# Performance work log

Hardware: AMD Instinct MI355X
Metric: run time of the kernel (lower is better)

## Reference

```python
import jax, jax.numpy as jnp
import numpy as np

NEG_INF = -1e30
EPS = 1e-7  # keras epsilon used by K.ctc_batch_cost


def setup_inputs() -> dict:
    key = jax.random.key(0)
    k1, k2 = jax.random.split(key)
    B, T, C, L = 1024, 256, 128, 32
    logits = jax.random.normal(k1, (B, T, C), dtype=jnp.float32)
    y_pred = jax.nn.softmax(logits, axis=-1)  # ctc_batch_cost expects probabilities
    y_true = jax.random.randint(k2, (B, L), 0, 126, dtype=jnp.int64)
    return {"y_true": y_true, "y_pred": y_pred}


def _ctc_batch_cost(y_true, y_pred):
    # Faithful to K.ctc_batch_cost with input_length=T, label_length=L, blank=C-1
    B, T, C = y_pred.shape
    L = y_true.shape[1]
    blank = C - 1
    S = 2 * L + 1
    logp = jnp.log(y_pred + EPS)  # [B,T,C]

    # extended label sequence: blank, l0, blank, l1, ..., blank  -> [B,S]
    ext = jnp.full((B, S), blank, dtype=jnp.int32)
    ext = ext.at[:, 1::2].set(y_true.astype(jnp.int32))

    # emission log-probs along extended labels: [B,T,S]
    lp_ext = jnp.take_along_axis(logp, ext[:, None, :], axis=2)

    # s-2 skip allowed only for non-blank labels differing from label two back
    is_blank = ext == blank
    same2 = jnp.concatenate(
        [jnp.ones((B, 2), bool), ext[:, 2:] == ext[:, :-2]], axis=1)
    skip_add = jnp.where(is_blank | same2, NEG_INF, 0.0)  # [B,S]

    alpha0 = jnp.full((B, S), NEG_INF, dtype=logp.dtype)
    alpha0 = alpha0.at[:, 0].set(lp_ext[:, 0, 0])
    alpha0 = alpha0.at[:, 1].set(lp_ext[:, 0, 1])

    def shift(x, n):
        return jnp.pad(x, ((0, 0), (n, 0)), constant_values=NEG_INF)[:, :S]

    def step(alpha, lp_t):
        a0 = alpha
        a1 = shift(alpha, 1)
        a2 = jnp.maximum(shift(alpha, 2) + skip_add, NEG_INF)
        m = jnp.maximum(jnp.maximum(a0, a1), a2)
        lse = m + jnp.log(jnp.exp(a0 - m) + jnp.exp(a1 - m) + jnp.exp(a2 - m))
        new = jnp.maximum(lse + lp_t, NEG_INF)
        return new, None

    lp_ext_t = jnp.swapaxes(lp_ext, 0, 1)  # [T,B,S]
    alpha_T, _ = jax.lax.scan(step, alpha0, lp_ext_t[1:])
    final = jnp.logaddexp(alpha_T[:, S - 1], alpha_T[:, S - 2])  # [B]
    return -final[:, None]  # [B,1] like ctc_batch_cost


def reference(y_true, y_pred):
    return _ctc_batch_cost(y_true, y_pred)
```

## Files before the change

kernel.cpp:

```cpp
#include <hip/hip_runtime.h>
#include <hip/hip_bf16.h>


#define CTC_B 1024
#define CTC_T 256
#define CTC_C 128
#define CTC_L 32
#define CTC_BLANK 127
#define CTC_EPS 1e-7f

#define KSTRIDE 130
#define TABSZ  (34 * KSTRIDE)

#define DPP_WAVE_SHL1 0x130
#define DPP_WAVE_SHR1 0x138

__device__ __forceinline__ double bperm_f64(int addr, double v) {
    union { double d; int i[2]; } u; u.d = v;
    int x = __builtin_amdgcn_ds_bpermute(addr, u.i[0]);
    int y = __builtin_amdgcn_ds_bpermute(addr, u.i[1]);
    union { int i[2]; double d; } r; r.i[0] = x; r.i[1] = y;
    return r.d;
}

__device__ __forceinline__ double dpp_shr1_f64(double v) {
    union { double d; int i[2]; } u; u.d = v;
    int x = __builtin_amdgcn_update_dpp(0, u.i[0], DPP_WAVE_SHR1, 0xF, 0xF, true);
    int y = __builtin_amdgcn_update_dpp(0, u.i[1], DPP_WAVE_SHR1, 0xF, 0xF, true);
    union { int i[2]; double d; } r; r.i[0] = x; r.i[1] = y;
    return r.d;
}

__device__ __forceinline__ double dpp_shl1_f64(double v) {
    union { double d; int i[2]; } u; u.d = v;
    int x = __builtin_amdgcn_update_dpp(0, u.i[0], DPP_WAVE_SHL1, 0xF, 0xF, true);
    int y = __builtin_amdgcn_update_dpp(0, u.i[1], DPP_WAVE_SHL1, 0xF, 0xF, true);
    union { int i[2]; double d; } r; r.i[0] = x; r.i[1] = y;
    return r.d;
}

__device__ __forceinline__ double bcast0_f64(double v) {
    union { double d; int i[2]; } u; u.d = v;
    int x = __builtin_amdgcn_readfirstlane(u.i[0]);
    int y = __builtin_amdgcn_readfirstlane(u.i[1]);
    union { int i[2]; double d; } r; r.i[0] = x; r.i[1] = y;
    return r.d;
}

__global__ __launch_bounds__(256) void ctc_loss_kernel(
    const int* __restrict__ y_true,
    const float* __restrict__ y_pred,
    float* __restrict__ out)
{
    __shared__ float tabs[2 * TABSZ];
    float* Ftab = tabs;
    float* Btab = tabs + TABSZ;

    const int b = blockIdx.x;
    const int tid = threadIdx.x;
    const int lane = tid & 63;
    const int wave = tid >> 6;

    const float* yp = y_pred + (size_t)b * CTC_T * CTC_C;

    int lbl = CTC_BLANK;
    if (lane < CTC_L) lbl = y_true[b * CTC_L + lane];

    {
        const int t0 = wave * 64;
        const int src_addr = (lbl >> 1) << 2;
        const bool odd = (lbl & 1) != 0;
        float* tab = (wave < 2) ? Ftab : Btab;
        #pragma unroll 8
        for (int k = 0; k < 64; ++k) {
            const int t = t0 + k;
            const float2 r =
                *reinterpret_cast<const float2*>(yp + (size_t)t * CTC_C + 2 * lane);
            union { float f; int i; } c0, c1;
            c0.f = r.x; c1.f = r.y;
            int g0 = __builtin_amdgcn_ds_bpermute(src_addr, c0.i);
            int g1 = __builtin_amdgcn_ds_bpermute(src_addr, c1.i);
            union { int i; float f; } s0, s1;
            s0.i = g0; s1.i = g1;
            float p = odd ? s1.f : s0.f;
            float v = (lane == 33) ? 0.0f : (p + CTC_EPS) * 128.0f;
            const int idx = (wave < 2) ? ((t + 127) & 127) : (255 - t);
            if (lane <= 33) tab[lane * KSTRIDE + idx] = v;
        }
    }
    __syncthreads();

    if (wave != 0) return;

    double skip = 0.0;
    if (lane >= 1 && lane < CTC_L) {
        if (y_true[b * CTC_L + lane - 1] != lbl) skip = 1.0;
    }
    double skipn = 0.0;
    if (lane <= 30) {
        if (y_true[b * CTC_L + lane + 1] != lbl) skipn = 1.0;
    } else if (lane == 32) {
        skipn = 1.0;
    }

    const int lidx = (lane < 32) ? lane : 32;
    const int pv_idx = (lane < 32) ? lane : 33;
    const int tn = (lane <= 30) ? (lane + 1)
                 : (lane == 31) ? 33
                 : (lane == 32) ? 0
                 : 32;
    const int pbi = (lane == 32) ? 33 : 32;
    const bool is32 = (lane == 32);

    const float* Fpv = Ftab + pv_idx * KSTRIDE;
    const float* Fpb = Ftab + 32 * KSTRIDE;
    const float* Bpa = Btab + lidx * KSTRIDE;
    const float* Bp1 = Btab + tn * KSTRIDE;
    const float* Bpb = Btab + pbi * KSTRIDE;

    double lo = 0.0, hi = 0.0;
    if (lane == 0) {
        lo = (double)Ftab[32 * KSTRIDE + 127];
        hi = (double)Ftab[0 * KSTRIDE + 127];
    }
    double a = 0.0, bb = 0.0;
    if (lane == 31) { a = 1.0; bb = 1.0; }

#define STEP(pvf, pbf, paf, pa1f, pbbf) {                       \
        double ph  = dpp_shr1_f64(hi);                          \
        double a1s = dpp_shl1_f64(a);                           \
        double a1  = is32 ? bcast0_f64(a) : a1s;                \
        double nl = (lo + ph) * (double)(pbf);                  \
        double nh = (hi + lo + skip * ph) * (double)(pvf);      \
        double v  = (double)(pa1f) * a1;                        \
        double u  = (double)(pbbf) * bb;                        \
        double nb = u + v;                                      \
        double na = fma((double)(paf), a, fma(skipn, v, u));    \
        lo = nl; hi = nh; a = na; bb = nb;                      \
    }

#define LD2(p, o) (*reinterpret_cast<const float2*>((p) + (o)))

    float2 c_pv0 = LD2(Fpv, 0), c_pv1 = LD2(Fpv, 2);
    float2 c_pb0 = LD2(Fpb, 0), c_pb1 = LD2(Fpb, 2);
    float2 c_pa0 = LD2(Bpa, 0), c_pa1 = LD2(Bpa, 2);
    float2 c_p10 = LD2(Bp1, 0), c_p11 = LD2(Bp1, 2);
    float2 c_pb0b = LD2(Bpb, 0), c_pb1b = LD2(Bpb, 2);

    for (int g = 0; g < 31; ++g) {
        const int o = 4 * (g + 1);
        float2 n_pv0 = LD2(Fpv, o), n_pv1 = LD2(Fpv, o + 2);
        float2 n_pb0 = LD2(Fpb, o), n_pb1 = LD2(Fpb, o + 2);
        float2 n_pa0 = LD2(Bpa, o), n_pa1 = LD2(Bpa, o + 2);
        float2 n_p10 = LD2(Bp1, o), n_p11 = LD2(Bp1, o + 2);
        float2 n_pb0b = LD2(Bpb, o), n_pb1b = LD2(Bpb, o + 2);

        STEP(c_pv0.x, c_pb0.x, c_pa0.x, c_p10.x, c_pb0b.x);
        STEP(c_pv0.y, c_pb0.y, c_pa0.y, c_p10.y, c_pb0b.y);
        STEP(c_pv1.x, c_pb1.x, c_pa1.x, c_p11.x, c_pb1b.x);
        STEP(c_pv1.y, c_pb1.y, c_pa1.y, c_p11.y, c_pb1b.y);

        c_pv0 = n_pv0; c_pv1 = n_pv1;
        c_pb0 = n_pb0; c_pb1 = n_pb1;
        c_pa0 = n_pa0; c_pa1 = n_pa1;
        c_p10 = n_p10; c_p11 = n_p11;
        c_pb0b = n_pb0b; c_pb1b = n_pb1b;
    }

    STEP(c_pv0.x, c_pb0.x, c_pa0.x, c_p10.x, c_pb0b.x);
    STEP(c_pv0.y, c_pb0.y, c_pa0.y, c_p10.y, c_pb0b.y);
    STEP(c_pv1.x, c_pb1.x, c_pa1.x, c_p11.x, c_pb1b.x);

    {
        double a1s = dpp_shl1_f64(a);
        double a1  = is32 ? bcast0_f64(a) : a1s;
        double v  = (double)c_p11.y * a1;
        double u  = (double)c_pb1b.y * bb;
        double nb = u + v;
        double na = fma((double)c_pa1.y, a, fma(skipn, v, u));
        a = na; bb = nb;
    }

#undef STEP
#undef LD2

    double beA = bperm_f64(32 << 2, a);
    double beB = bperm_f64(((lane + 63) & 63) << 2, bb);
    double be = (lane == 0) ? beA : beB;
    double partial = (lane <= 32) ? (lo * be + hi * a) : 0.0;
    #pragma unroll
    for (int off = 32; off >= 1; off >>= 1)
        partial += __shfl_down(partial, off);
    if (lane == 0) {
        out[b] = (float)(1242.1197475634219 - log(partial));
    }
}

extern "C" void kernel_launch(void* const* d_in, const int* in_sizes, int n_in,
                              void* d_out, int out_size, void* d_ws, size_t ws_size,
                              hipStream_t stream) {
    const int*   y_true = (const int*)d_in[0];
    const float* y_pred = (const float*)d_in[1];
    float*       out    = (float*)d_out;

    ctc_loss_kernel<<<CTC_B, 256, 0, stream>>>(y_true, y_pred, out);
}
```

Baseline: 212.5 us.

## Split CTC into gather kernel and 64-thread scan kernel via workspace

Splits the fused kernel in two. The first kernel gathers the label emission probabilities into a global workspace, using two blocks per batch item. The second kernel runs the forward/backward recurrence with one 64-thread wave per batch item and reads its probabilities from global memory (L2) instead of LDS. The aim is to stop three idle waves holding a block's LDS during the serial scan, raise occupancy, and overlap the scan across more batches. The cost is a second launch plus a round trip to global memory for about 37 MB of gathered data, with a fallback to the old fused kernel when the workspace is too small.

```diff
diff --git a/kernel.cpp b/kernel.cpp
--- a/kernel.cpp
+++ b/kernel.cpp
@@ -9,8 +9,9 @@
 #define CTC_BLANK 127
 #define CTC_EPS 1e-7f
 
-#define KSTRIDE 130
-#define TABSZ  (34 * KSTRIDE)
+#define ROWS 36
+#define PROB_DW (CTC_T * ROWS)
+#define WS_NEED ((size_t)CTC_B * PROB_DW * 4)
 
 #define DPP_WAVE_SHL1 0x130
 #define DPP_WAVE_SHR1 0x138
@@ -46,6 +47,171 @@
     union { int i[2]; double d; } r; r.i[0] = x; r.i[1] = y;
     return r.d;
 }
+
+__global__ __launch_bounds__(256) void ctc_phase1_kernel(
+    const int* __restrict__ y_true,
+    const float* __restrict__ y_pred,
+    float* __restrict__ ws)
+{
+    __shared__ float lp[128 * ROWS];
+
+    const int blk = blockIdx.x;
+    const int b = blk >> 1;
+    const int half = blk & 1;
+    const int tid = threadIdx.x;
+    const int lane = tid & 63;
+    const int wave = tid >> 6;
+
+    const float* yp = y_pred + (size_t)b * CTC_T * CTC_C;
+
+    int lbl = CTC_BLANK;
+    if (lane < CTC_L) lbl = y_true[b * CTC_L + lane];
+
+    const int tbase = half * 128;
+    const int t0 = tbase + wave * 32;
+    const int src_addr = (lbl >> 1) << 2;
+    const bool odd = (lbl & 1) != 0;
+
+    #pragma unroll 8
+    for (int k = 0; k < 32; ++k) {
+        const int t = t0 + k;
+        const float2 r =
+            *reinterpret_cast<const float2*>(yp + (size_t)t * CTC_C + 2 * lane);
+        union { float f; int i; } c0, c1;
+        c0.f = r.x; c1.f = r.y;
+        int g0 = __builtin_amdgcn_ds_bpermute(src_addr, c0.i);
+        int g1 = __builtin_amdgcn_ds_bpermute(src_addr, c1.i);
+        union { int i; float f; } s0, s1;
+        s0.i = g0; s1.i = g1;
+        float p = odd ? s1.f : s0.f;
+        float v = (lane == 33) ? 0.0f : (p + CTC_EPS) * 128.0f;
+        if (lane <= 33) lp[(t - tbase) * ROWS + lane] = v;
+    }
+    __syncthreads();
+
+    const int4* src = reinterpret_cast<const int4*>(lp);
+    int4* dst = reinterpret_cast<int4*>(ws + (size_t)b * PROB_DW + (size_t)tbase * ROWS);
+    #pragma unroll
+    for (int i = 0; i < 5; ++i) {
+        const int q = tid + i * 256;
+        if (q < 1152) dst[q] = src[q];
+    }
+}
+
+__global__ __launch_bounds__(64) void ctc_scan_kernel(
+    const int* __restrict__ y_true,
+    const float* __restrict__ ws,
+    float* __restrict__ out)
+{
+    const int b = blockIdx.x;
+    const int lane = threadIdx.x;
+    const float* tab = ws + (size_t)b * PROB_DW;
+
+    int lbl = CTC_BLANK;
+    if (lane < CTC_L) lbl = y_true[b * CTC_L + lane];
+
+    double skip = 0.0;
+    if (lane >= 1 && lane < CTC_L) {
+        if (y_true[b * CTC_L + lane - 1] != lbl) skip = 1.0;
+    }
+    double skipn = 0.0;
+    if (lane <= 30) {
+        if (y_true[b * CTC_L + lane + 1] != lbl) skipn = 1.0;
+    } else if (lane == 32) {
+        skipn = 1.0;
+    }
+
+    const int lidx = (lane < 32) ? lane : 32;
+    const int pv_idx = (lane < 32) ? lane : 33;
+    const int tn = (lane <= 30) ? (lane + 1)
+                 : (lane == 31) ? 33
+                 : (lane == 32) ? 0
+                 : 32;
+    const int pbi = (lane == 32) ? 33 : 32;
+    const bool is32 = (lane == 32);
+
+    double lo = 0.0, hi = 0.0;
+    if (lane == 0) {
+        lo = (double)tab[32];
+        hi = (double)tab[0];
+    }
+    double a = 0.0, bb = 0.0;
+    if (lane == 31) { a = 1.0; bb = 1.0; }
+
+#define STEP(pvf, pbf, paf, pa1f, pbbf) {                       \
+        double ph  = dpp_shr1_f64(hi);                          \
+        double a1s = dpp_shl1_f64(a);                           \
+        double a1  = is32 ? bcast0_f64(a) : a1s;                \
+        double nl = (lo + ph) * (double)(pbf);                  \
+        double nh = (hi + lo + skip * ph) * (double)(pvf);      \
+        double v  = (double)(pa1f) * a1;                        \
+        double u  = (double)(pbbf) * bb;                        \
+        double nb = u + v;                                      \
+        double na = fma((double)(paf), a, fma(skipn, v, u));    \
+        lo = nl; hi = nh; a = na; bb = nb;                      \
+    }
+
+    float cpv[4], cpb[4], cpa[4], cp1[4], cpbb[4];
+    float npv[4], npb[4], npa[4], np1[4], npbb[4];
+
+    #pragma unroll
+    for (int j = 0; j < 4; ++j) {
+        const float* rf = tab + (size_t)(1 + j) * ROWS;
+        const float* rb = tab + (size_t)(255 - j) * ROWS;
+        cpv[j] = rf[pv_idx]; cpb[j] = rf[32];
+        cpa[j] = rb[lidx];   cp1[j] = rb[tn]; cpbb[j] = rb[pbi];
+    }
+
+    for (int g = 0; g < 31; ++g) {
+        #pragma unroll
+        for (int j = 0; j < 4; ++j) {
+            const int kk = 4 * (g + 1) + j;
+            const float* rf = tab + (size_t)(1 + kk) * ROWS;
+            const float* rb = tab + (size_t)(255 - kk) * ROWS;
+            npv[j] = rf[pv_idx]; npb[j] = rf[32];
+            npa[j] = rb[lidx];   np1[j] = rb[tn]; npbb[j] = rb[pbi];
+        }
+        __builtin_amdgcn_sched_barrier(0);
+        #pragma unroll
+        for (int j = 0; j < 4; ++j)
+            STEP(cpv[j], cpb[j], cpa[j], cp1[j], cpbb[j]);
+        __builtin_amdgcn_sched_barrier(0);
+        #pragma unroll
+        for (int j = 0; j < 4; ++j) {
+            cpv[j] = npv[j]; cpb[j] = npb[j];
+            cpa[j] = npa[j]; cp1[j] = np1[j]; cpbb[j] = npbb[j];
+        }
+    }
+
+    STEP(cpv[0], cpb[0], cpa[0], cp1[0], cpbb[0]);
+    STEP(cpv[1], cpb[1], cpa[1], cp1[1], cpbb[1]);
+    STEP(cpv[2], cpb[2], cpa[2], cp1[2], cpbb[2]);
+
+    {
+        double a1s = dpp_shl1_f64(a);
+        double a1  = is32 ? bcast0_f64(a) : a1s;
+        double v  = (double)cp1[3] * a1;
+        double u  = (double)cpbb[3] * bb;
+        double nb = u + v;
+        double na = fma((double)cpa[3], a, fma(skipn, v, u));
+        a = na; bb = nb;
+    }
+#undef STEP
+
+    double beA = bperm_f64(32 << 2, a);
+    double beB = bperm_f64(((lane + 63) & 63) << 2, bb);
+    double be = (lane == 0) ? beA : beB;
+    double partial = (lane <= 32) ? (lo * be + hi * a) : 0.0;
+    #pragma unroll
+    for (int off = 32; off >= 1; off >>= 1)
+        partial += __shfl_down(partial, off);
+    if (lane == 0) {
+        out[b] = (float)(1242.1197475634219 - log(partial));
+    }
+}
+
+#define KSTRIDE 130
+#define TABSZ  (34 * KSTRIDE)
 
 __global__ __launch_bounds__(256) void ctc_loss_kernel(
     const int* __restrict__ y_true,
@@ -139,50 +305,24 @@
         lo = nl; hi = nh; a = na; bb = nb;                      \
     }
 
-#define LD2(p, o) (*reinterpret_cast<const float2*>((p) + (o)))
-
-    float2 c_pv0 = LD2(Fpv, 0), c_pv1 = LD2(Fpv, 2);
-    float2 c_pb0 = LD2(Fpb, 0), c_pb1 = LD2(Fpb, 2);
-    float2 c_pa0 = LD2(Bpa, 0), c_pa1 = LD2(Bpa, 2);
-    float2 c_p10 = LD2(Bp1, 0), c_p11 = LD2(Bp1, 2);
-    float2 c_pb0b = LD2(Bpb, 0), c_pb1b = LD2(Bpb, 2);
-
-    for (int g = 0; g < 31; ++g) {
-        const int o = 4 * (g + 1);
-        float2 n_pv0 = LD2(Fpv, o), n_pv1 = LD2(Fpv, o + 2);
-        float2 n_pb0 = LD2(Fpb, o), n_pb1 = LD2(Fpb, o + 2);
-        float2 n_pa0 = LD2(Bpa, o), n_pa1 = LD2(Bpa, o + 2);
-        float2 n_p10 = LD2(Bp1, o), n_p11 = LD2(Bp1, o + 2);
-        float2 n_pb0b = LD2(Bpb, o), n_pb1b = LD2(Bpb, o + 2);
-
-        STEP(c_pv0.x, c_pb0.x, c_pa0.x, c_p10.x, c_pb0b.x);
-        STEP(c_pv0.y, c_pb0.y, c_pa0.y, c_p10.y, c_pb0b.y);
-        STEP(c_pv1.x, c_pb1.x, c_pa1.x, c_p11.x, c_pb1b.x);
-        STEP(c_pv1.y, c_pb1.y, c_pa1.y, c_p11.y, c_pb1b.y);
-
-        c_pv0 = n_pv0; c_pv1 = n_pv1;
-        c_pb0 = n_pb0; c_pb1 = n_pb1;
-        c_pa0 = n_pa0; c_pa1 = n_pa1;
-        c_p10 = n_p10; c_p11 = n_p11;
-        c_pb0b = n_pb0b; c_pb1b = n_pb1b;
-    }
-
-    STEP(c_pv0.x, c_pb0.x, c_pa0.x, c_p10.x, c_pb0b.x);
-    STEP(c_pv0.y, c_pb0.y, c_pa0.y, c_p10.y, c_pb0b.y);
-    STEP(c_pv1.x, c_pb1.x, c_pa1.x, c_p11.x, c_pb1b.x);
-
+    for (int k = 0; k < 127; ++k) {
+        float pvf  = Fpv[k];
+        float pbf  = Fpb[k];
+        float paf  = Bpa[k];
+        float pa1f = Bp1[k];
+        float pbbf = Bpb[k];
+        STEP(pvf, pbf, paf, pa1f, pbbf);
+    }
     {
         double a1s = dpp_shl1_f64(a);
         double a1  = is32 ? bcast0_f64(a) : a1s;
-        double v  = (double)c_p11.y * a1;
-        double u  = (double)c_pb1b.y * bb;
+        double v  = (double)Bp1[127] * a1;
+        double u  = (double)Bpb[127] * bb;
         double nb = u + v;
-        double na = fma((double)c_pa1.y, a, fma(skipn, v, u));
+        double na = fma((double)Bpa[127], a, fma(skipn, v, u));
         a = na; bb = nb;
     }
-
 #undef STEP
-#undef LD2
 
     double beA = bperm_f64(32 << 2, a);
     double beB = bperm_f64(((lane + 63) & 63) << 2, bb);
@@ -203,5 +343,11 @@
     const float* y_pred = (const float*)d_in[1];
     float*       out    = (float*)d_out;
 
-    ctc_loss_kernel<<<CTC_B, 256, 0, stream>>>(y_true, y_pred, out);
-}
+    if (d_ws != nullptr && ws_size >= WS_NEED) {
+        float* ws = (float*)d_ws;
+        ctc_phase1_kernel<<<2 * CTC_B, 256, 0, stream>>>(y_true, y_pred, ws);
+        ctc_scan_kernel<<<CTC_B, 64, 0, stream>>>(y_true, ws, out);
+    } else {
+        ctc_loss_kernel<<<CTC_B, 256, 0, stream>>>(y_true, y_pred, out);
+    }
+}
```

New measurement: 214.3 us. No clear change (+0.9%).
